# Performance work log

Measured on AMD Instinct MI355X. Metric: run time of the kernel, lower is better.

## Reference

```python
import jax, jax.numpy as jnp
import numpy as np

N, D = 8192, 64


def setup_inputs() -> dict:
    key = jax.random.key(0)
    X = jax.random.normal(key, (N, D), dtype=jnp.float32)
    return {"X": X}


def reference(X):
    # Pairwise Euclidean distance matrix d_X[i, j] = ||X[i] - X[j]||_2.
    # Same math as sqrt(sum((X[:,None,:] - X[None,:,:])**2, -1)) but computed
    # via the Gram-matrix identity to avoid the [N, N, D] intermediate.
    sq_norms = jnp.sum(X * X, axis=1)                      # [N]
    gram = jnp.einsum('id,jd->ij', X, X)                   # [N, N]
    sq = sq_norms[:, None] + sq_norms[None, :] - 2.0 * gram
    sq = jnp.maximum(sq, 0.0)                              # clamp fp round-off
    # safe sqrt: exact zeros (diagonal) stay 0 with finite grad
    pos = sq > 0.0
    d_X = jnp.where(pos, jnp.sqrt(jnp.where(pos, sq, 1.0)), 0.0)
    return d_X
```

## Files before the change

kernel.cpp:

```cpp
#include <hip/hip_runtime.h>

#define NN 8192
#define DD 64

typedef short bf16x8 __attribute__((ext_vector_type(8)));
typedef float f32x4 __attribute__((ext_vector_type(4)));

__device__ __forceinline__ unsigned short f2bf(float f) {
    unsigned int u = __float_as_uint(f);
    unsigned int r = (u + 0x7FFFu + ((u >> 16) & 1u)) >> 16;
    return (unsigned short)r;
}

__device__ __forceinline__ float fsqrt(float x) {
#if __has_builtin(__builtin_amdgcn_sqrtf)
    return __builtin_amdgcn_sqrtf(x);
#else
    return sqrtf(x);
#endif
}

__global__ __launch_bounds__(256) void rips_setup(const float* __restrict__ X,
                                                  unsigned short* __restrict__ Xb,
                                                  float* __restrict__ norms) {
    const int t   = blockIdx.x * 256 + threadIdx.x;
    const int row = t >> 3;
    const int j   = t & 7;
    const float* p = X + (size_t)row * DD + j * 8;
    float4 lo = *(const float4*)p;
    float4 hi = *(const float4*)(p + 4);

    bf16x8 v;
    v[0] = (short)f2bf(lo.x); v[1] = (short)f2bf(lo.y);
    v[2] = (short)f2bf(lo.z); v[3] = (short)f2bf(lo.w);
    v[4] = (short)f2bf(hi.x); v[5] = (short)f2bf(hi.y);
    v[6] = (short)f2bf(hi.z); v[7] = (short)f2bf(hi.w);
    *(bf16x8*)(Xb + (size_t)row * DD + j * 8) = v;

    float acc = lo.x*lo.x + lo.y*lo.y + lo.z*lo.z + lo.w*lo.w
              + hi.x*hi.x + hi.y*hi.y + hi.z*hi.z + hi.w*hi.w;
    acc += __shfl_xor(acc, 1);
    acc += __shfl_xor(acc, 2);
    acc += __shfl_xor(acc, 4);
    if (j == 0) norms[row] = acc;
}

__global__ __launch_bounds__(256) void rips_main(const unsigned short* __restrict__ Xb,
                                                 const float* __restrict__ norms,
                                                 float* __restrict__ out) {
    const int bid = blockIdx.x;
    const int rowBase = (bid >> 4) * 32;
    const int colBase = (bid & 15) * 512;

    const int tid  = threadIdx.x;
    const int lane = tid & 63;
    const int wc   = tid >> 6;

    __shared__ float rn[32];
    __shared__ float cn[512];
    __shared__ float stage[4][16 * 132];

    if (tid < 32) rn[tid] = norms[rowBase + tid];
    cn[tid]       = norms[colBase + tid];
    cn[tid + 256] = norms[colBase + tid + 256];
    __syncthreads();

    const int fr = lane & 15;
    const int kg = lane >> 4;

    const bool tileHasDiag = (rowBase >= colBase) && (rowBase < colBase + 512);

    f32x4 acc[2][8];
    #pragma unroll
    for (int m = 0; m < 2; ++m)
        #pragma unroll
        for (int n = 0; n < 8; ++n)
            acc[m][n] = (f32x4){0.f, 0.f, 0.f, 0.f};

    #pragma unroll
    for (int kk = 0; kk < DD; kk += 32) {
        bf16x8 a[8], b[2];
        #pragma unroll
        for (int n = 0; n < 8; ++n)
            a[n] = *(const bf16x8*)(Xb + (size_t)(colBase + wc * 128 + n * 16 + fr) * DD + kk + kg * 8);
        #pragma unroll
        for (int m = 0; m < 2; ++m)
            b[m] = *(const bf16x8*)(Xb + (size_t)(rowBase + m * 16 + fr) * DD + kk + kg * 8);
        #pragma unroll
        for (int m = 0; m < 2; ++m)
            #pragma unroll
            for (int n = 0; n < 8; ++n)
                acc[m][n] = __builtin_amdgcn_mfma_f32_16x16x32_bf16(a[n], b[m], acc[m][n], 0, 0, 0);
    }

    float* st = stage[wc];
    const int sr = lane >> 5;
    const int sc = lane & 31;

    #pragma unroll
    for (int m = 0; m < 2; ++m) {
        const int grow  = rowBase + m * 16 + fr;
        const float rnv = rn[m * 16 + fr];
        #pragma unroll
        for (int n = 0; n < 8; ++n) {
            const int col_l = wc * 128 + n * 16 + kg * 4;
            const int gcol0 = colBase + col_l;
            const float4 cnv = *(const float4*)&cn[col_l];
            f32x4 o;
            o[0] = fsqrt(fmaxf(rnv + cnv.x - 2.0f * acc[m][n][0], 0.0f));
            o[1] = fsqrt(fmaxf(rnv + cnv.y - 2.0f * acc[m][n][1], 0.0f));
            o[2] = fsqrt(fmaxf(rnv + cnv.z - 2.0f * acc[m][n][2], 0.0f));
            o[3] = fsqrt(fmaxf(rnv + cnv.w - 2.0f * acc[m][n][3], 0.0f));
            if (tileHasDiag) {
                if (grow == gcol0 + 0) o[0] = 0.0f;
                if (grow == gcol0 + 1) o[1] = 0.0f;
                if (grow == gcol0 + 2) o[2] = 0.0f;
                if (grow == gcol0 + 3) o[3] = 0.0f;
            }
            *(f32x4*)&st[fr * 132 + n * 16 + kg * 4] = o;
        }
        #pragma unroll
        for (int t = 0; t < 8; ++t) {
            const int R = t * 2 + sr;
            f32x4 v = *(const f32x4*)&st[R * 132 + sc * 4];
            const int srow = rowBase + m * 16 + R;
            const int scol = colBase + wc * 128 + sc * 4;
            *(f32x4*)(out + (size_t)srow * NN + scol) = v;
        }
    }
}

__global__ __launch_bounds__(256) void rips_fallback(const float* __restrict__ X,
                                                     float* __restrict__ out) {
    const int rowBase = blockIdx.y * 128;
    const int colBase = blockIdx.x * 128;
    const int tid  = threadIdx.x;
    const int lane = tid & 63;
    const int w    = tid >> 6;
    const int wr   = w >> 1;
    const int wc   = w & 1;

    __shared__ float rn[128];
    __shared__ float cn[128];
    {
        const int idx  = tid & 127;
        const int base = (tid < 128) ? rowBase : colBase;
        const float4* p = (const float4*)(X + (size_t)(base + idx) * DD);
        float acc = 0.0f;
        #pragma unroll
        for (int i = 0; i < 16; ++i) {
            float4 v = p[i];
            acc += v.x * v.x + v.y * v.y + v.z * v.z + v.w * v.w;
        }
        if (tid < 128) rn[idx] = acc;
        else           cn[idx] = acc;
    }
    __syncthreads();

    f32x4 acc[4][4];
    #pragma unroll
    for (int m = 0; m < 4; ++m)
        #pragma unroll
        for (int n = 0; n < 4; ++n)
            acc[m][n] = (f32x4){0.f, 0.f, 0.f, 0.f};

    const int fr = lane & 15;
    const int kg = lane >> 4;

    #pragma unroll
    for (int kk = 0; kk < DD; kk += 32) {
        bf16x8 a[4], b[4];
        #pragma unroll
        for (int m = 0; m < 4; ++m) {
            const float* p = X + (size_t)(rowBase + wr * 64 + m * 16 + fr) * DD + kk + kg * 8;
            float4 lo = *(const float4*)p;
            float4 hi = *(const float4*)(p + 4);
            bf16x8 t;
            t[0] = (short)f2bf(lo.x); t[1] = (short)f2bf(lo.y);
            t[2] = (short)f2bf(lo.z); t[3] = (short)f2bf(lo.w);
            t[4] = (short)f2bf(hi.x); t[5] = (short)f2bf(hi.y);
            t[6] = (short)f2bf(hi.z); t[7] = (short)f2bf(hi.w);
            a[m] = t;
        }
        #pragma unroll
        for (int n = 0; n < 4; ++n) {
            const float* p = X + (size_t)(colBase + wc * 64 + n * 16 + fr) * DD + kk + kg * 8;
            float4 lo = *(const float4*)p;
            float4 hi = *(const float4*)(p + 4);
            bf16x8 t;
            t[0] = (short)f2bf(lo.x); t[1] = (short)f2bf(lo.y);
            t[2] = (short)f2bf(lo.z); t[3] = (short)f2bf(lo.w);
            t[4] = (short)f2bf(hi.x); t[5] = (short)f2bf(hi.y);
            t[6] = (short)f2bf(hi.z); t[7] = (short)f2bf(hi.w);
            b[n] = t;
        }
        #pragma unroll
        for (int m = 0; m < 4; ++m)
            #pragma unroll
            for (int n = 0; n < 4; ++n)
                acc[m][n] = __builtin_amdgcn_mfma_f32_16x16x32_bf16(a[m], b[n], acc[m][n], 0, 0, 0);
    }

    #pragma unroll
    for (int m = 0; m < 4; ++m) {
        #pragma unroll
        for (int n = 0; n < 4; ++n) {
            #pragma unroll
            for (int r = 0; r < 4; ++r) {
                const int row_l = wr * 64 + m * 16 + kg * 4 + r;
                const int col_l = wc * 64 + n * 16 + fr;
                const float g  = acc[m][n][r];
                float sq = rn[row_l] + cn[col_l] - 2.0f * g;
                sq = fmaxf(sq, 0.0f);
                float dv = sqrtf(sq);
                const int grow = rowBase + row_l;
                const int gcol = colBase + col_l;
                if (grow == gcol) dv = 0.0f;
                out[(size_t)grow * NN + gcol] = dv;
            }
        }
    }
}

extern "C" void kernel_launch(void* const* d_in, const int* in_sizes, int n_in,
                              void* d_out, int out_size, void* d_ws, size_t ws_size,
                              hipStream_t stream) {
    const float* X = (const float*)d_in[0];
    float* out = (float*)d_out;

    const size_t xb_bytes   = (size_t)NN * DD * sizeof(unsigned short);
    const size_t norm_bytes = (size_t)NN * sizeof(float);

    if (ws_size >= xb_bytes + norm_bytes) {
        unsigned short* Xb = (unsigned short*)d_ws;
        float* norms = (float*)((char*)d_ws + xb_bytes);
        rips_setup<<<dim3(NN * 8 / 256, 1, 1), dim3(256, 1, 1), 0, stream>>>(X, Xb, norms);
        rips_main<<<dim3((NN / 32) * (NN / 512), 1, 1), dim3(256, 1, 1), 0, stream>>>(Xb, norms, out);
    } else {
        dim3 grid(NN / 128, NN / 128, 1);
        rips_fallback<<<grid, dim3(256, 1, 1), 0, stream>>>(X, out);
    }
}
```

Before: 65.19 us.

## Restructure main kernel into row stripes with per-wave column loop

```diff
diff --git a/kernel.cpp b/kernel.cpp
--- a/kernel.cpp
+++ b/kernel.cpp
@@ -45,87 +45,80 @@
     if (j == 0) norms[row] = acc;
 }
 
-__global__ __launch_bounds__(256) void rips_main(const unsigned short* __restrict__ Xb,
-                                                 const float* __restrict__ norms,
-                                                 float* __restrict__ out) {
-    const int bid = blockIdx.x;
-    const int rowBase = (bid >> 4) * 32;
-    const int colBase = (bid & 15) * 512;
-
+__global__ __launch_bounds__(512) void rips_stripe(const unsigned short* __restrict__ Xb,
+                                                   const float* __restrict__ norms,
+                                                   float* __restrict__ out) {
+    const int rowBase = blockIdx.x * 16;
     const int tid  = threadIdx.x;
     const int lane = tid & 63;
-    const int wc   = tid >> 6;
-
-    __shared__ float rn[32];
-    __shared__ float cn[512];
-    __shared__ float stage[4][16 * 132];
-
-    if (tid < 32) rn[tid] = norms[rowBase + tid];
-    cn[tid]       = norms[colBase + tid];
-    cn[tid + 256] = norms[colBase + tid + 256];
-    __syncthreads();
+    const int w    = tid >> 6;
 
     const int fr = lane & 15;
     const int kg = lane >> 4;
 
-    const bool tileHasDiag = (rowBase >= colBase) && (rowBase < colBase + 512);
-
-    f32x4 acc[2][8];
-    #pragma unroll
-    for (int m = 0; m < 2; ++m)
-        #pragma unroll
-        for (int n = 0; n < 8; ++n)
-            acc[m][n] = (f32x4){0.f, 0.f, 0.f, 0.f};
-
-    #pragma unroll
-    for (int kk = 0; kk < DD; kk += 32) {
-        bf16x8 a[8], b[2];
-        #pragma unroll
-        for (int n = 0; n < 8; ++n)
-            a[n] = *(const bf16x8*)(Xb + (size_t)(colBase + wc * 128 + n * 16 + fr) * DD + kk + kg * 8);
-        #pragma unroll
-        for (int m = 0; m < 2; ++m)
-            b[m] = *(const bf16x8*)(Xb + (size_t)(rowBase + m * 16 + fr) * DD + kk + kg * 8);
-        #pragma unroll
-        for (int m = 0; m < 2; ++m)
-            #pragma unroll
-            for (int n = 0; n < 8; ++n)
-                acc[m][n] = __builtin_amdgcn_mfma_f32_16x16x32_bf16(a[n], b[m], acc[m][n], 0, 0, 0);
-    }
-
-    float* st = stage[wc];
-    const int sr = lane >> 5;
-    const int sc = lane & 31;
-
-    #pragma unroll
-    for (int m = 0; m < 2; ++m) {
-        const int grow  = rowBase + m * 16 + fr;
-        const float rnv = rn[m * 16 + fr];
-        #pragma unroll
-        for (int n = 0; n < 8; ++n) {
-            const int col_l = wc * 128 + n * 16 + kg * 4;
-            const int gcol0 = colBase + col_l;
-            const float4 cnv = *(const float4*)&cn[col_l];
-            f32x4 o;
-            o[0] = fsqrt(fmaxf(rnv + cnv.x - 2.0f * acc[m][n][0], 0.0f));
-            o[1] = fsqrt(fmaxf(rnv + cnv.y - 2.0f * acc[m][n][1], 0.0f));
-            o[2] = fsqrt(fmaxf(rnv + cnv.z - 2.0f * acc[m][n][2], 0.0f));
-            o[3] = fsqrt(fmaxf(rnv + cnv.w - 2.0f * acc[m][n][3], 0.0f));
-            if (tileHasDiag) {
-                if (grow == gcol0 + 0) o[0] = 0.0f;
-                if (grow == gcol0 + 1) o[1] = 0.0f;
-                if (grow == gcol0 + 2) o[2] = 0.0f;
-                if (grow == gcol0 + 3) o[3] = 0.0f;
+    __shared__ float stage[8][16 * 68];
+    float* st = stage[w];
+
+    const bf16x8 b0 = *(const bf16x8*)(Xb + (size_t)(rowBase + fr) * DD + 0  + kg * 8);
+    const bf16x8 b1 = *(const bf16x8*)(Xb + (size_t)(rowBase + fr) * DD + 32 + kg * 8);
+    const float rnv = norms[rowBase + fr];
+
+    const int sr = lane >> 4;
+    const int sc = lane & 15;
+
+    for (int c = 0; c < 8; ++c) {
+        const int colBase = w * 1024 + c * 128;
+        const bool hasDiag = ((rowBase >> 7) == (colBase >> 7));
+
+        f32x4 acc[8];
+        #pragma unroll
+        for (int n = 0; n < 8; ++n) acc[n] = (f32x4){0.f, 0.f, 0.f, 0.f};
+
+        {
+            bf16x8 a[8];
+            #pragma unroll
+            for (int n = 0; n < 8; ++n)
+                a[n] = *(const bf16x8*)(Xb + (size_t)(colBase + n * 16 + fr) * DD + 0 + kg * 8);
+            #pragma unroll
+            for (int n = 0; n < 8; ++n)
+                acc[n] = __builtin_amdgcn_mfma_f32_16x16x32_bf16(a[n], b0, acc[n], 0, 0, 0);
+            #pragma unroll
+            for (int n = 0; n < 8; ++n)
+                a[n] = *(const bf16x8*)(Xb + (size_t)(colBase + n * 16 + fr) * DD + 32 + kg * 8);
+            #pragma unroll
+            for (int n = 0; n < 8; ++n)
+                acc[n] = __builtin_amdgcn_mfma_f32_16x16x32_bf16(a[n], b1, acc[n], 0, 0, 0);
+        }
+
+        const int grow = rowBase + fr;
+        #pragma unroll
+        for (int h = 0; h < 2; ++h) {
+            #pragma unroll
+            for (int nn = 0; nn < 4; ++nn) {
+                const int idx   = h * 4 + nn;
+                const int gcol0 = colBase + idx * 16 + kg * 4;
+                const float4 cnv = *(const float4*)(norms + gcol0);
+                f32x4 o;
+                o[0] = fsqrt(fmaxf(rnv + cnv.x - 2.0f * acc[idx][0], 0.0f));
+                o[1] = fsqrt(fmaxf(rnv + cnv.y - 2.0f * acc[idx][1], 0.0f));
+                o[2] = fsqrt(fmaxf(rnv + cnv.z - 2.0f * acc[idx][2], 0.0f));
+                o[3] = fsqrt(fmaxf(rnv + cnv.w - 2.0f * acc[idx][3], 0.0f));
+                if (hasDiag) {
+                    if (grow == gcol0 + 0) o[0] = 0.0f;
+                    if (grow == gcol0 + 1) o[1] = 0.0f;
+                    if (grow == gcol0 + 2) o[2] = 0.0f;
+                    if (grow == gcol0 + 3) o[3] = 0.0f;
+                }
+                *(f32x4*)&st[fr * 68 + nn * 16 + kg * 4] = o;
             }
-            *(f32x4*)&st[fr * 132 + n * 16 + kg * 4] = o;
-        }
-        #pragma unroll
-        for (int t = 0; t < 8; ++t) {
-            const int R = t * 2 + sr;
-            f32x4 v = *(const f32x4*)&st[R * 132 + sc * 4];
-            const int srow = rowBase + m * 16 + R;
-            const int scol = colBase + wc * 128 + sc * 4;
-            *(f32x4*)(out + (size_t)srow * NN + scol) = v;
+            #pragma unroll
+            for (int t = 0; t < 4; ++t) {
+                const int R = t * 4 + sr;
+                f32x4 v = *(const f32x4*)&st[R * 68 + sc * 4];
+                const int srow = rowBase + R;
+                const int scol = colBase + h * 64 + sc * 4;
+                *(f32x4*)(out + (size_t)srow * NN + scol) = v;
+            }
         }
     }
 }
@@ -235,7 +228,7 @@
         unsigned short* Xb = (unsigned short*)d_ws;
         float* norms = (float*)((char*)d_ws + xb_bytes);
         rips_setup<<<dim3(NN * 8 / 256, 1, 1), dim3(256, 1, 1), 0, stream>>>(X, Xb, norms);
-        rips_main<<<dim3((NN / 32) * (NN / 512), 1, 1), dim3(256, 1, 1), 0, stream>>>(Xb, norms, out);
+        rips_stripe<<<dim3(NN / 16, 1, 1), dim3(512, 1, 1), 0, stream>>>(Xb, norms, out);
     } else {
         dim3 grid(NN / 128, NN / 128, 1);
         rips_fallback<<<grid, dim3(256, 1, 1), 0, stream>>>(X, out);
```

Result: slower. 87.46 us (+34.2%).
